# Kernel tuning notes

Measured on AMD Instinct MI355X. Metric: run time of the kernel, lower is better.

The kernel has to match this reference:

```python
import jax, jax.numpy as jnp
import numpy as np

N = 100000
E = 3200000
D = 128


def setup_inputs() -> dict:
    key = jax.random.key(0)
    k1, k2, k3, k4 = jax.random.split(key, 4)
    x = jax.random.normal(k1, (N, D), dtype=jnp.float32)
    edge_index = jax.random.randint(k2, (2, E), 0, N, dtype=jnp.int64)
    W1 = jax.random.normal(k3, (D, 16), dtype=jnp.float32) * (1.0 / np.sqrt(D))
    b1 = jnp.zeros((16,), dtype=jnp.float32)
    W2 = jax.random.normal(k4, (16, 2), dtype=jnp.float32) * (1.0 / np.sqrt(16))
    b2 = jnp.zeros((2,), dtype=jnp.float32)
    return {"x": x, "edge_index": edge_index, "W1": W1, "b1": b1, "W2": W2, "b2": b2}


def _gcn_conv(h, src, dst, norm, W, b):
    # transform first (out_dim <= in_dim), then normalized scatter-add aggregation
    h = h @ W                                   # [N, out]
    msg = h[src] * norm[:, None]                # [E+N, out] gathered messages
    agg = jax.ops.segment_sum(msg, dst, num_segments=N)
    return agg + b


def reference(x, edge_index, W1, b1, W2, b2):
    loops = jnp.arange(N, dtype=edge_index.dtype)
    src = jnp.concatenate([edge_index[0], loops])   # row (message source)
    dst = jnp.concatenate([edge_index[1], loops])   # col (aggregation target)
    # symmetric GCN normalization: deg over dst, norm = d^-1/2[src] * d^-1/2[dst]
    deg = jax.ops.segment_sum(jnp.ones_like(src, dtype=x.dtype), dst, num_segments=N)
    dinv = jnp.where(deg > 0, jax.lax.rsqrt(deg), 0.0)
    norm = dinv[src] * dinv[dst]

    h = _gcn_conv(x, src, dst, norm, W1, b1)
    h = jax.nn.relu(h)
    h = _gcn_conv(h, src, dst, norm, W2, b2)
    return jax.nn.log_softmax(h, axis=1)
```

## Files before the change

kernel.cpp:

```cpp
#include <hip/hip_runtime.h>
#include <hip/hip_fp16.h>
#include <math.h>

#define N_NODES 100000
#define N_EDGES 3200000
#define D_IN    128
#define H1      16

#define PSH     8
#define NPB     200
#define NB      500
#define CAP     9936
#define PBLK    512
#define CHUNK   6250
#define ELS_CAP 13760
#define NLINES  (ELS_CAP / 16)
#define MROWS   64

__device__ __forceinline__ unsigned bkt(int d) {
    return (unsigned)(((unsigned long long)(unsigned)d * 671089ull) >> 27);
}


__global__ __launch_bounds__(512) void k_partition(const int* __restrict__ ei,
                                                   int* __restrict__ cursor,
                                                   unsigned int* __restrict__ eop) {
    __shared__ int h[512];
    __shared__ int loff[512];
    __shared__ int resv[NB];
    __shared__ int wsum[8], wpre[8];
    __shared__ unsigned short owner[NLINES];
    __shared__ unsigned char rank8[CHUNK];
    __shared__ unsigned int els[ELS_CAP];
    int t = threadIdx.x;
    h[t] = 0;
    __syncthreads();
    int c0 = blockIdx.x * CHUNK;
    const int2* s2 = (const int2*)(ei + c0);
    const int2* d2 = (const int2*)(ei + N_EDGES + c0);
    for (int i = t; i < CHUNK / 2; i += 512) {
        int2 dd = d2[i];
        rank8[2 * i]     = (unsigned char)atomicAdd(&h[bkt(dd.x)], 1);
        rank8[2 * i + 1] = (unsigned char)atomicAdd(&h[bkt(dd.y)], 1);
    }
    __syncthreads();
    int cp = (h[t] + 15) & ~15;
    int lane = t & 63, w = t >> 6;
    int v = cp;
#pragma unroll
    for (int o = 1; o < 64; o <<= 1) {
        int u = __shfl_up(v, o);
        if (lane >= o) v += u;
    }
    if (lane == 63) wsum[w] = v;
    __syncthreads();
    if (t < 8) {
        int s = wsum[t];
#pragma unroll
        for (int o = 1; o < 8; o <<= 1) {
            int u = __shfl_up(s, o);
            if (t >= o) s += u;
        }
        wpre[t] = s;
    }
    __syncthreads();
    int inc = v + ((w > 0) ? wpre[w - 1] : 0);
    int totalpad = wpre[7];
    int ex = inc - cp;
    loff[t] = ex;
    if (t < NB && cp) {
        resv[t] = atomicAdd(&cursor[t], cp);
        int l0 = ex >> 4;
        for (int k = 0; k < (cp >> 4); ++k) owner[l0 + k] = (unsigned short)t;
    }
    for (int i = t; i < totalpad; i += 512) els[i] = 0xFFFFFFFFu;
    __syncthreads();
    for (int i = t; i < CHUNK / 2; i += 512) {
        int2 ss = s2[i];
        int2 dd = d2[i];
        unsigned bx = bkt(dd.x), by = bkt(dd.y);
        els[loff[bx] + (int)rank8[2 * i]] =
            ((unsigned)ss.x << PSH) | (unsigned)(dd.x - (int)(bx * NPB));
        els[loff[by] + (int)rank8[2 * i + 1]] =
            ((unsigned)ss.y << PSH) | (unsigned)(dd.y - (int)(by * NPB));
    }
    __syncthreads();
    for (int i = t; i < totalpad; i += 512) {
        int b   = owner[i >> 4];
        int pos = resv[b] + (i - loff[b]);
        if (pos < CAP)
            eop[(size_t)b * CAP + pos] = els[i];
    }
}

__global__ __launch_bounds__(512) void k_build(const int* __restrict__ cursor,
                                               unsigned int* __restrict__ eop,
                                               int* __restrict__ nstart,
                                               int* __restrict__ ndeg,
                                               float* __restrict__ dinv) {
    __shared__ unsigned int els[CAP];
    __shared__ int cnt[256];
    __shared__ int off[256];
    __shared__ int wsum[4], wpre[4];
    int t = threadIdx.x, b = blockIdx.x;
    if (t < 256) cnt[t] = 0;
    __syncthreads();
    int n = cursor[b]; if (n > CAP) n = CAP;
    unsigned int* reg = eop + (size_t)b * CAP;
    for (int i4 = t; i4 < (n >> 2); i4 += 512) {
        uint4 wv = ((const uint4*)reg)[i4];
        unsigned int e0 = wv.x, e1 = wv.y, e2 = wv.z, e3 = wv.w;
        int r;
        if ((int)e0 >= 0) { r = atomicAdd(&cnt[e0 & 0xFF], 1); e0 |= (unsigned)r << 25; }
        if ((int)e1 >= 0) { r = atomicAdd(&cnt[e1 & 0xFF], 1); e1 |= (unsigned)r << 25; }
        if ((int)e2 >= 0) { r = atomicAdd(&cnt[e2 & 0xFF], 1); e2 |= (unsigned)r << 25; }
        if ((int)e3 >= 0) { r = atomicAdd(&cnt[e3 & 0xFF], 1); e3 |= (unsigned)r << 25; }
        ((uint4*)els)[i4] = make_uint4(e0, e1, e2, e3);
    }
    __syncthreads();
    int lane = t & 63, w = t >> 6;
    int v = 0;
    if (t < 256) {
        v = cnt[t];
#pragma unroll
        for (int o = 1; o < 64; o <<= 1) {
            int u = __shfl_up(v, o);
            if (lane >= o) v += u;
        }
        if (lane == 63) wsum[w] = v;
    }
    __syncthreads();
    if (t < 4) {
        int s = wsum[t];
#pragma unroll
        for (int o = 1; o < 4; o <<= 1) {
            int u = __shfl_up(s, o);
            if (t >= o) s += u;
        }
        wpre[t] = s;
    }
    __syncthreads();
    if (t < 256) {
        int val = cnt[t];
        int ex = (v + ((w > 0) ? wpre[w - 1] : 0)) - val;
        off[t] = ex;
        if (t < NPB) {
            int node = b * NPB + t;
            nstart[node] = b * CAP + ex;
            ndeg[node]   = val;
            dinv[node]   = rsqrtf((float)(val + 1));
        }
    }
    __syncthreads();
    for (int i4 = t; i4 < (n >> 2); i4 += 512) {
        uint4 wv = ((const uint4*)els)[i4];
        unsigned int e; unsigned s;
        e = wv.x; s = (e >> PSH) & 0x1FFFFu;
        if (s < N_NODES) reg[off[e & 0xFF] + (int)(e >> 25)] = s;
        e = wv.y; s = (e >> PSH) & 0x1FFFFu;
        if (s < N_NODES) reg[off[e & 0xFF] + (int)(e >> 25)] = s;
        e = wv.z; s = (e >> PSH) & 0x1FFFFu;
        if (s < N_NODES) reg[off[e & 0xFF] + (int)(e >> 25)] = s;
        e = wv.w; s = (e >> PSH) & 0x1FFFFu;
        if (s < N_NODES) reg[off[e & 0xFF] + (int)(e >> 25)] = s;
    }
}

__global__ __launch_bounds__(256) void k_mm1(const float* __restrict__ x,
                                             const float* __restrict__ W1,
                                             const float* __restrict__ dinv,
                                             __half* __restrict__ h1h) {
    __shared__ float sX[MROWS][D_IN + 1];
    int t = threadIdx.x;
    int r0 = blockIdx.x * MROWS;
    for (int i = t; i < MROWS * (D_IN / 4); i += 256) {
        int row = i >> 5, c4 = i & 31;
        int grow = r0 + row;
        float4 v = (grow < N_NODES) ? ((const float4*)x)[(size_t)grow * 32 + c4]
                                    : make_float4(0.f, 0.f, 0.f, 0.f);
        sX[row][c4 * 4 + 0] = v.x; sX[row][c4 * 4 + 1] = v.y;
        sX[row][c4 * 4 + 2] = v.z; sX[row][c4 * 4 + 3] = v.w;
    }
    __syncthreads();
    int lane = t & 63;
    int c0 = __builtin_amdgcn_readfirstlane((t >> 6) * 4);
    float a0 = 0.f, a1 = 0.f, a2 = 0.f, a3 = 0.f;
#pragma unroll 4
    for (int d = 0; d < D_IN; ++d) {
        float xv = sX[lane][d];
        a0 = fmaf(xv, W1[d * 16 + c0 + 0], a0);
        a1 = fmaf(xv, W1[d * 16 + c0 + 1], a1);
        a2 = fmaf(xv, W1[d * 16 + c0 + 2], a2);
        a3 = fmaf(xv, W1[d * 16 + c0 + 3], a3);
    }
    int grow = r0 + lane;
    if (grow < N_NODES) {
        float di = dinv[grow];
        __half2* o = (__half2*)(h1h + (size_t)grow * H1 + c0);
        o[0] = __floats2half2_rn(a0 * di, a1 * di);
        o[1] = __floats2half2_rn(a2 * di, a3 * di);
    }
}

__global__ __launch_bounds__(256) void k_agg1(const unsigned int* __restrict__ eop,
                                              const int* __restrict__ nstart,
                                              const int* __restrict__ ndeg,
                                              const __half* __restrict__ h1h,
                                              const float* __restrict__ dinv,
                                              const float* __restrict__ b1,
                                              const float* __restrict__ W2,
                                              float2* __restrict__ h2f) {
    int t = threadIdx.x;
    int g = t >> 3, l = t & 7;
    int base = (t & 63) & ~7;
    int node = blockIdx.x * 32 + g;
    int e0 = nstart[node], deg = ndeg[node];
    const __half2* H = (const __half2*)h1h;
    float a0 = 0.f, a1 = 0.f, c0 = 0.f, c1 = 0.f;
    int nfull = deg & ~7;
    int j = e0;
    for (; j < e0 + nfull; j += 8) {
        int s = (int)eop[j + l];
#pragma unroll
        for (int k = 0; k < 8; k += 2) {
            int sk0 = __shfl(s, base + k);
            int sk1 = __shfl(s, base + k + 1);
            float2 f0 = __half22float2(H[sk0 * 8 + l]);
            float2 f1 = __half22float2(H[sk1 * 8 + l]);
            a0 += f0.x; a1 += f0.y;
            c0 += f1.x; c1 += f1.y;
        }
    }
    int r = e0 + deg - j;
    if (r) {
        int s = (l < r) ? (int)eop[j + l] : -1;
#pragma unroll
        for (int k = 0; k < 8; ++k) {
            int sk = __shfl(s, base + k);
            int su = (sk >= 0) ? sk : 0;
            float m = (sk >= 0) ? 1.f : 0.f;
            float2 f = __half22float2(H[su * 8 + l]);
            a0 = fmaf(f.x, m, a0); a1 = fmaf(f.y, m, a1);
        }
    }
    float di = dinv[node];
    float2 self = __half22float2(H[node * 8 + l]);
    float s0 = (a0 + c0) + self.x, s1 = (a1 + c1) + self.y;
    float2 bb = ((const float2*)b1)[l];
    float h0 = fmaxf(fmaf(di, s0, bb.x), 0.f);
    float h1v = fmaxf(fmaf(di, s1, bb.y), 0.f);
    float4 wv = ((const float4*)W2)[l];
    float p0 = h0 * wv.x + h1v * wv.z;
    float p1 = h0 * wv.y + h1v * wv.w;
#pragma unroll
    for (int off = 1; off < 8; off <<= 1) {
        p0 += __shfl_xor(p0, off);
        p1 += __shfl_xor(p1, off);
    }
    if (l == 0) h2f[node] = make_float2(p0 * di, p1 * di);
}

__global__ __launch_bounds__(256) void k_agg2(const unsigned int* __restrict__ eop,
                                              const int* __restrict__ nstart,
                                              const int* __restrict__ ndeg,
                                              const float2* __restrict__ h2f,
                                              const float* __restrict__ dinv,
                                              const float* __restrict__ b2,
                                              float* __restrict__ out) {
    int tg = blockIdx.x * 256 + threadIdx.x;
    int node = tg >> 2, l = tg & 3;
    if (node >= N_NODES) return;
    int e0 = nstart[node], e1 = e0 + ndeg[node];
    float ax = 0.f, ay = 0.f;
    for (int j = e0 + l; j < e1; j += 4) {
        float2 m = h2f[eop[j]];
        ax += m.x; ay += m.y;
    }
    ax += __shfl_xor(ax, 1); ay += __shfl_xor(ay, 1);
    ax += __shfl_xor(ax, 2); ay += __shfl_xor(ay, 2);
    if (l == 0) {
        float di = dinv[node];
        float2 self = h2f[node];
        float a0 = fmaf(di, ax + self.x, b2[0]);
        float a1 = fmaf(di, ay + self.y, b2[1]);
        float m  = fmaxf(a0, a1);
        float lg = logf(expf(a0 - m) + expf(a1 - m));
        out[2 * node]     = a0 - m - lg;
        out[2 * node + 1] = a1 - m - lg;
    }
}

extern "C" void kernel_launch(void* const* d_in, const int* in_sizes, int n_in,
                              void* d_out, int out_size, void* d_ws, size_t ws_size,
                              hipStream_t stream) {
    const float* x  = (const float*)d_in[0];
    const int*   ei = (const int*)d_in[1];
    const float* W1 = (const float*)d_in[2];
    const float* b1 = (const float*)d_in[3];
    const float* W2 = (const float*)d_in[4];
    const float* b2 = (const float*)d_in[5];
    float* out = (float*)d_out;

    int*          cursor = (int*)d_ws;
    int*          nstart = cursor + 512;
    int*          ndeg   = nstart + 100352;
    float*        dinv   = (float*)(ndeg + 100352);
    __half*       h1h    = (__half*)(dinv + 100352);
    float2*       h2f    = (float2*)(h1h + (size_t)100352 * H1);
    unsigned int* eop    = (unsigned int*)(h2f + 100352);

    hipMemsetAsync(cursor, 0, 512 * sizeof(int), stream);
    k_partition<<<PBLK, 512, 0, stream>>>(ei, cursor, eop);
    k_build    <<<NB,   512, 0, stream>>>(cursor, eop, nstart, ndeg, dinv);
    k_mm1      <<<(N_NODES + MROWS - 1) / MROWS, 256, 0, stream>>>(x, W1, dinv, h1h);
    k_agg1     <<<N_NODES / 32, 256, 0, stream>>>(eop, nstart, ndeg, h1h, dinv, b1, W2, h2f);
    k_agg2     <<<(N_NODES * 4 + 255) / 256, 256, 0, stream>>>(eop, nstart, ndeg, h2f, dinv, b2, out);
}
```

Before: 204.0 us.

## Fuse partition and build into one cooperative kernel with grid sync

Merges the edge-partition and per-bucket build kernels into a single cooperative kernel. A grid-wide barrier now separates the two phases instead of a kernel boundary, and both phases share one shared-memory union. The aim is to remove one launch and its inter-kernel gap. In exchange, all 512 blocks must be co-resident, and the grid sync plus the raised occupancy hint may cost some throughput.

```diff
diff --git a/kernel.cpp b/kernel.cpp
--- a/kernel.cpp
+++ b/kernel.cpp
@@ -1,6 +1,9 @@
 #include <hip/hip_runtime.h>
+#include <hip/hip_cooperative_groups.h>
 #include <hip/hip_fp16.h>
 #include <math.h>
+
+namespace cg = cooperative_groups;
 
 #define N_NODES 100000
 #define N_EDGES 3200000
@@ -22,147 +25,159 @@
 }
 
 
-__global__ __launch_bounds__(512) void k_partition(const int* __restrict__ ei,
-                                                   int* __restrict__ cursor,
-                                                   unsigned int* __restrict__ eop) {
-    __shared__ int h[512];
-    __shared__ int loff[512];
-    __shared__ int resv[NB];
-    __shared__ int wsum[8], wpre[8];
-    __shared__ unsigned short owner[NLINES];
-    __shared__ unsigned char rank8[CHUNK];
-    __shared__ unsigned int els[ELS_CAP];
+struct PShared {
+    int h[512];
+    int loff[512];
+    int resv[NB];
+    int wsum[8], wpre[8];
+    unsigned short owner[NLINES];
+    unsigned char rank8[CHUNK];
+    unsigned int els[ELS_CAP];
+};
+struct BShared {
+    unsigned int els[CAP];
+    int cnt[256];
+    int off[256];
+    int wsum[4], wpre[4];
+};
+union SortShared { PShared p; BShared b; };
+
+__global__ __launch_bounds__(512, 4) void k_sort(const int* __restrict__ ei,
+                                                 int* __restrict__ cursor,
+                                                 unsigned int* __restrict__ eop,
+                                                 int* __restrict__ nstart,
+                                                 int* __restrict__ ndeg,
+                                                 float* __restrict__ dinv) {
+    __shared__ SortShared sm;
     int t = threadIdx.x;
-    h[t] = 0;
-    __syncthreads();
-    int c0 = blockIdx.x * CHUNK;
-    const int2* s2 = (const int2*)(ei + c0);
-    const int2* d2 = (const int2*)(ei + N_EDGES + c0);
-    for (int i = t; i < CHUNK / 2; i += 512) {
-        int2 dd = d2[i];
-        rank8[2 * i]     = (unsigned char)atomicAdd(&h[bkt(dd.x)], 1);
-        rank8[2 * i + 1] = (unsigned char)atomicAdd(&h[bkt(dd.y)], 1);
-    }
-    __syncthreads();
-    int cp = (h[t] + 15) & ~15;
-    int lane = t & 63, w = t >> 6;
-    int v = cp;
-#pragma unroll
-    for (int o = 1; o < 64; o <<= 1) {
-        int u = __shfl_up(v, o);
-        if (lane >= o) v += u;
-    }
-    if (lane == 63) wsum[w] = v;
-    __syncthreads();
-    if (t < 8) {
-        int s = wsum[t];
-#pragma unroll
-        for (int o = 1; o < 8; o <<= 1) {
-            int u = __shfl_up(s, o);
-            if (t >= o) s += u;
-        }
-        wpre[t] = s;
-    }
-    __syncthreads();
-    int inc = v + ((w > 0) ? wpre[w - 1] : 0);
-    int totalpad = wpre[7];
-    int ex = inc - cp;
-    loff[t] = ex;
-    if (t < NB && cp) {
-        resv[t] = atomicAdd(&cursor[t], cp);
-        int l0 = ex >> 4;
-        for (int k = 0; k < (cp >> 4); ++k) owner[l0 + k] = (unsigned short)t;
-    }
-    for (int i = t; i < totalpad; i += 512) els[i] = 0xFFFFFFFFu;
-    __syncthreads();
-    for (int i = t; i < CHUNK / 2; i += 512) {
-        int2 ss = s2[i];
-        int2 dd = d2[i];
-        unsigned bx = bkt(dd.x), by = bkt(dd.y);
-        els[loff[bx] + (int)rank8[2 * i]] =
-            ((unsigned)ss.x << PSH) | (unsigned)(dd.x - (int)(bx * NPB));
-        els[loff[by] + (int)rank8[2 * i + 1]] =
-            ((unsigned)ss.y << PSH) | (unsigned)(dd.y - (int)(by * NPB));
-    }
-    __syncthreads();
-    for (int i = t; i < totalpad; i += 512) {
-        int b   = owner[i >> 4];
-        int pos = resv[b] + (i - loff[b]);
-        if (pos < CAP)
-            eop[(size_t)b * CAP + pos] = els[i];
-    }
-}
-
-__global__ __launch_bounds__(512) void k_build(const int* __restrict__ cursor,
-                                               unsigned int* __restrict__ eop,
-                                               int* __restrict__ nstart,
-                                               int* __restrict__ ndeg,
-                                               float* __restrict__ dinv) {
-    __shared__ unsigned int els[CAP];
-    __shared__ int cnt[256];
-    __shared__ int off[256];
-    __shared__ int wsum[4], wpre[4];
-    int t = threadIdx.x, b = blockIdx.x;
-    if (t < 256) cnt[t] = 0;
-    __syncthreads();
-    int n = cursor[b]; if (n > CAP) n = CAP;
-    unsigned int* reg = eop + (size_t)b * CAP;
-    for (int i4 = t; i4 < (n >> 2); i4 += 512) {
-        uint4 wv = ((const uint4*)reg)[i4];
-        unsigned int e0 = wv.x, e1 = wv.y, e2 = wv.z, e3 = wv.w;
-        int r;
-        if ((int)e0 >= 0) { r = atomicAdd(&cnt[e0 & 0xFF], 1); e0 |= (unsigned)r << 25; }
-        if ((int)e1 >= 0) { r = atomicAdd(&cnt[e1 & 0xFF], 1); e1 |= (unsigned)r << 25; }
-        if ((int)e2 >= 0) { r = atomicAdd(&cnt[e2 & 0xFF], 1); e2 |= (unsigned)r << 25; }
-        if ((int)e3 >= 0) { r = atomicAdd(&cnt[e3 & 0xFF], 1); e3 |= (unsigned)r << 25; }
-        ((uint4*)els)[i4] = make_uint4(e0, e1, e2, e3);
-    }
-    __syncthreads();
-    int lane = t & 63, w = t >> 6;
-    int v = 0;
-    if (t < 256) {
-        v = cnt[t];
+
+    {
+        sm.p.h[t] = 0;
+        __syncthreads();
+        int c0 = blockIdx.x * CHUNK;
+        const int2* s2 = (const int2*)(ei + c0);
+        const int2* d2 = (const int2*)(ei + N_EDGES + c0);
+        for (int i = t; i < CHUNK / 2; i += 512) {
+            int2 dd = d2[i];
+            sm.p.rank8[2 * i]     = (unsigned char)atomicAdd(&sm.p.h[bkt(dd.x)], 1);
+            sm.p.rank8[2 * i + 1] = (unsigned char)atomicAdd(&sm.p.h[bkt(dd.y)], 1);
+        }
+        __syncthreads();
+        int cp = (sm.p.h[t] + 15) & ~15;
+        int lane = t & 63, w = t >> 6;
+        int v = cp;
 #pragma unroll
         for (int o = 1; o < 64; o <<= 1) {
             int u = __shfl_up(v, o);
             if (lane >= o) v += u;
         }
-        if (lane == 63) wsum[w] = v;
-    }
-    __syncthreads();
-    if (t < 4) {
-        int s = wsum[t];
-#pragma unroll
-        for (int o = 1; o < 4; o <<= 1) {
-            int u = __shfl_up(s, o);
-            if (t >= o) s += u;
-        }
-        wpre[t] = s;
-    }
-    __syncthreads();
-    if (t < 256) {
-        int val = cnt[t];
-        int ex = (v + ((w > 0) ? wpre[w - 1] : 0)) - val;
-        off[t] = ex;
-        if (t < NPB) {
-            int node = b * NPB + t;
-            nstart[node] = b * CAP + ex;
-            ndeg[node]   = val;
-            dinv[node]   = rsqrtf((float)(val + 1));
-        }
-    }
-    __syncthreads();
-    for (int i4 = t; i4 < (n >> 2); i4 += 512) {
-        uint4 wv = ((const uint4*)els)[i4];
-        unsigned int e; unsigned s;
-        e = wv.x; s = (e >> PSH) & 0x1FFFFu;
-        if (s < N_NODES) reg[off[e & 0xFF] + (int)(e >> 25)] = s;
-        e = wv.y; s = (e >> PSH) & 0x1FFFFu;
-        if (s < N_NODES) reg[off[e & 0xFF] + (int)(e >> 25)] = s;
-        e = wv.z; s = (e >> PSH) & 0x1FFFFu;
-        if (s < N_NODES) reg[off[e & 0xFF] + (int)(e >> 25)] = s;
-        e = wv.w; s = (e >> PSH) & 0x1FFFFu;
-        if (s < N_NODES) reg[off[e & 0xFF] + (int)(e >> 25)] = s;
+        if (lane == 63) sm.p.wsum[w] = v;
+        __syncthreads();
+        if (t < 8) {
+            int s = sm.p.wsum[t];
+#pragma unroll
+            for (int o = 1; o < 8; o <<= 1) {
+                int u = __shfl_up(s, o);
+                if (t >= o) s += u;
+            }
+            sm.p.wpre[t] = s;
+        }
+        __syncthreads();
+        int inc = v + ((w > 0) ? sm.p.wpre[w - 1] : 0);
+        int totalpad = sm.p.wpre[7];
+        int ex = inc - cp;
+        sm.p.loff[t] = ex;
+        if (t < NB && cp) {
+            sm.p.resv[t] = atomicAdd(&cursor[t], cp);
+            int l0 = ex >> 4;
+            for (int k = 0; k < (cp >> 4); ++k) sm.p.owner[l0 + k] = (unsigned short)t;
+        }
+        for (int i = t; i < totalpad; i += 512) sm.p.els[i] = 0xFFFFFFFFu;
+        __syncthreads();
+        for (int i = t; i < CHUNK / 2; i += 512) {
+            int2 ss = s2[i];
+            int2 dd = d2[i];
+            unsigned bx = bkt(dd.x), by = bkt(dd.y);
+            sm.p.els[sm.p.loff[bx] + (int)sm.p.rank8[2 * i]] =
+                ((unsigned)ss.x << PSH) | (unsigned)(dd.x - (int)(bx * NPB));
+            sm.p.els[sm.p.loff[by] + (int)sm.p.rank8[2 * i + 1]] =
+                ((unsigned)ss.y << PSH) | (unsigned)(dd.y - (int)(by * NPB));
+        }
+        __syncthreads();
+        for (int i = t; i < totalpad; i += 512) {
+            int b   = sm.p.owner[i >> 4];
+            int pos = sm.p.resv[b] + (i - sm.p.loff[b]);
+            if (pos < CAP)
+                eop[(size_t)b * CAP + pos] = sm.p.els[i];
+        }
+    }
+
+    __threadfence();
+    cg::this_grid().sync();
+
+    int b = blockIdx.x;
+    if (b < NB) {
+        if (t < 256) sm.b.cnt[t] = 0;
+        __syncthreads();
+        int n = cursor[b]; if (n > CAP) n = CAP;
+        unsigned int* reg = eop + (size_t)b * CAP;
+        for (int i4 = t; i4 < (n >> 2); i4 += 512) {
+            uint4 wv = ((const uint4*)reg)[i4];
+            unsigned int e0 = wv.x, e1 = wv.y, e2 = wv.z, e3 = wv.w;
+            int r;
+            if ((int)e0 >= 0) { r = atomicAdd(&sm.b.cnt[e0 & 0xFF], 1); e0 |= (unsigned)r << 25; }
+            if ((int)e1 >= 0) { r = atomicAdd(&sm.b.cnt[e1 & 0xFF], 1); e1 |= (unsigned)r << 25; }
+            if ((int)e2 >= 0) { r = atomicAdd(&sm.b.cnt[e2 & 0xFF], 1); e2 |= (unsigned)r << 25; }
+            if ((int)e3 >= 0) { r = atomicAdd(&sm.b.cnt[e3 & 0xFF], 1); e3 |= (unsigned)r << 25; }
+            ((uint4*)sm.b.els)[i4] = make_uint4(e0, e1, e2, e3);
+        }
+        __syncthreads();
+        int lane = t & 63, w = t >> 6;
+        int v = 0;
+        if (t < 256) {
+            v = sm.b.cnt[t];
+#pragma unroll
+            for (int o = 1; o < 64; o <<= 1) {
+                int u = __shfl_up(v, o);
+                if (lane >= o) v += u;
+            }
+            if (lane == 63) sm.b.wsum[w] = v;
+        }
+        __syncthreads();
+        if (t < 4) {
+            int s = sm.b.wsum[t];
+#pragma unroll
+            for (int o = 1; o < 4; o <<= 1) {
+                int u = __shfl_up(s, o);
+                if (t >= o) s += u;
+            }
+            sm.b.wpre[t] = s;
+        }
+        __syncthreads();
+        if (t < 256) {
+            int val = sm.b.cnt[t];
+            int ex = (v + ((w > 0) ? sm.b.wpre[w - 1] : 0)) - val;
+            sm.b.off[t] = ex;
+            if (t < NPB) {
+                int node = b * NPB + t;
+                nstart[node] = b * CAP + ex;
+                ndeg[node]   = val;
+                dinv[node]   = rsqrtf((float)(val + 1));
+            }
+        }
+        __syncthreads();
+        for (int i4 = t; i4 < (n >> 2); i4 += 512) {
+            uint4 wv = ((const uint4*)sm.b.els)[i4];
+            unsigned int e; unsigned s;
+            e = wv.x; s = (e >> PSH) & 0x1FFFFu;
+            if (s < N_NODES) reg[sm.b.off[e & 0xFF] + (int)(e >> 25)] = s;
+            e = wv.y; s = (e >> PSH) & 0x1FFFFu;
+            if (s < N_NODES) reg[sm.b.off[e & 0xFF] + (int)(e >> 25)] = s;
+            e = wv.z; s = (e >> PSH) & 0x1FFFFu;
+            if (s < N_NODES) reg[sm.b.off[e & 0xFF] + (int)(e >> 25)] = s;
+            e = wv.w; s = (e >> PSH) & 0x1FFFFu;
+            if (s < N_NODES) reg[sm.b.off[e & 0xFF] + (int)(e >> 25)] = s;
+        }
     }
 }
 
@@ -310,9 +325,17 @@
     unsigned int* eop    = (unsigned int*)(h2f + 100352);
 
     hipMemsetAsync(cursor, 0, 512 * sizeof(int), stream);
-    k_partition<<<PBLK, 512, 0, stream>>>(ei, cursor, eop);
-    k_build    <<<NB,   512, 0, stream>>>(cursor, eop, nstart, ndeg, dinv);
-    k_mm1      <<<(N_NODES + MROWS - 1) / MROWS, 256, 0, stream>>>(x, W1, dinv, h1h);
-    k_agg1     <<<N_NODES / 32, 256, 0, stream>>>(eop, nstart, ndeg, h1h, dinv, b1, W2, h2f);
-    k_agg2     <<<(N_NODES * 4 + 255) / 256, 256, 0, stream>>>(eop, nstart, ndeg, h2f, dinv, b2, out);
-}
+
+    {
+        const int*    a0 = ei;     int*   a1 = cursor;
+        unsigned int* a2 = eop;    int*   a3 = nstart;
+        int*          a4 = ndeg;   float* a5 = dinv;
+        void* ka[6] = { &a0, &a1, &a2, &a3, &a4, &a5 };
+        hipLaunchCooperativeKernel((const void*)k_sort, dim3(PBLK), dim3(512),
+                                   ka, 0, stream);
+    }
+
+    k_mm1 <<<(N_NODES + MROWS - 1) / MROWS, 256, 0, stream>>>(x, W1, dinv, h1h);
+    k_agg1<<<N_NODES / 32, 256, 0, stream>>>(eop, nstart, ndeg, h1h, dinv, b1, W2, h2f);
+    k_agg2<<<(N_NODES * 4 + 255) / 256, 256, 0, stream>>>(eop, nstart, ndeg, h2f, dinv, b2, out);
+}
```

Measured after the change: 350.1 us. 1.72x slower.

## Fuse X·W1 into partition kernel, apply dinv during aggregation, pad cursors

Applied to the files above, without the earlier changes.

The separate k_mm1 kernel is removed. The dense X·W1 product now runs at the tail of k_partition, reusing its shared-memory buffer, with each block handling 196 rows. The product is stored without the dinv scaling, since dinv is not known until k_build, so k_agg1 now gathers dinv[src] per edge and multiplies it in. Cursor counters are spread 32 ints apart to reduce atomic contention, and k_agg2 uses 8 lanes per node instead of 4. The trade is one fewer launch and overlap of the GEMM with partitioning, against an extra scattered dinv load per edge in agg1 and a longer partition kernel.

```diff
diff --git a/kernel.cpp b/kernel.cpp
--- a/kernel.cpp
+++ b/kernel.cpp
@@ -15,7 +15,8 @@
 #define CHUNK   6250
 #define ELS_CAP 13760
 #define NLINES  (ELS_CAP / 16)
-#define MROWS   64
+#define CSTRIDE 32
+#define MMR     196
 
 __device__ __forceinline__ unsigned bkt(int d) {
     return (unsigned)(((unsigned long long)(unsigned)d * 671089ull) >> 27);
@@ -24,7 +25,10 @@
 
 __global__ __launch_bounds__(512) void k_partition(const int* __restrict__ ei,
                                                    int* __restrict__ cursor,
-                                                   unsigned int* __restrict__ eop) {
+                                                   unsigned int* __restrict__ eop,
+                                                   const float* __restrict__ x,
+                                                   const float* __restrict__ W1,
+                                                   __half* __restrict__ h1u) {
     __shared__ int h[512];
     __shared__ int loff[512];
     __shared__ int resv[NB];
@@ -35,9 +39,9 @@
     int t = threadIdx.x;
     h[t] = 0;
     __syncthreads();
-    int c0 = blockIdx.x * CHUNK;
-    const int2* s2 = (const int2*)(ei + c0);
-    const int2* d2 = (const int2*)(ei + N_EDGES + c0);
+    int c0e = blockIdx.x * CHUNK;
+    const int2* s2 = (const int2*)(ei + c0e);
+    const int2* d2 = (const int2*)(ei + N_EDGES + c0e);
     for (int i = t; i < CHUNK / 2; i += 512) {
         int2 dd = d2[i];
         rank8[2 * i]     = (unsigned char)atomicAdd(&h[bkt(dd.x)], 1);
@@ -69,7 +73,7 @@
     int ex = inc - cp;
     loff[t] = ex;
     if (t < NB && cp) {
-        resv[t] = atomicAdd(&cursor[t], cp);
+        resv[t] = atomicAdd(&cursor[t * CSTRIDE], cp);
         int l0 = ex >> 4;
         for (int k = 0; k < (cp >> 4); ++k) owner[l0 + k] = (unsigned short)t;
     }
@@ -90,6 +94,35 @@
         int pos = resv[b] + (i - loff[b]);
         if (pos < CAP)
             eop[(size_t)b * CAP + pos] = els[i];
+    }
+
+    float (*sXf)[D_IN + 1] = (float (*)[D_IN + 1])els;
+    int cc = __builtin_amdgcn_readfirstlane(2 * w);
+    int rbase = blockIdx.x * MMR;
+    for (int p = 0; p < 4; ++p) {
+        int pb = rbase + p * 64;
+        __syncthreads();
+        for (int i = t; i < 64 * 32; i += 512) {
+            int row = i >> 5, c4 = i & 31;
+            int grow = pb + row;
+            float4 vv = (grow < N_NODES) ? ((const float4*)x)[(size_t)grow * 32 + c4]
+                                         : make_float4(0.f, 0.f, 0.f, 0.f);
+            sXf[row][c4 * 4 + 0] = vv.x; sXf[row][c4 * 4 + 1] = vv.y;
+            sXf[row][c4 * 4 + 2] = vv.z; sXf[row][c4 * 4 + 3] = vv.w;
+        }
+        __syncthreads();
+        int lrow = p * 64 + lane;
+        int grow = pb + lane;
+        if (lrow < MMR && grow < N_NODES) {
+            float a0 = 0.f, a1 = 0.f;
+#pragma unroll 4
+            for (int d = 0; d < D_IN; ++d) {
+                float xv = sXf[lane][d];
+                a0 = fmaf(xv, W1[d * 16 + cc], a0);
+                a1 = fmaf(xv, W1[d * 16 + cc + 1], a1);
+            }
+            ((__half2*)h1u)[(size_t)grow * 8 + w] = __floats2half2_rn(a0, a1);
+        }
     }
 }
 
@@ -105,7 +138,7 @@
     int t = threadIdx.x, b = blockIdx.x;
     if (t < 256) cnt[t] = 0;
     __syncthreads();
-    int n = cursor[b]; if (n > CAP) n = CAP;
+    int n = cursor[b * CSTRIDE]; if (n > CAP) n = CAP;
     unsigned int* reg = eop + (size_t)b * CAP;
     for (int i4 = t; i4 < (n >> 2); i4 += 512) {
         uint4 wv = ((const uint4*)reg)[i4];
@@ -166,46 +199,10 @@
     }
 }
 
-__global__ __launch_bounds__(256) void k_mm1(const float* __restrict__ x,
-                                             const float* __restrict__ W1,
-                                             const float* __restrict__ dinv,
-                                             __half* __restrict__ h1h) {
-    __shared__ float sX[MROWS][D_IN + 1];
-    int t = threadIdx.x;
-    int r0 = blockIdx.x * MROWS;
-    for (int i = t; i < MROWS * (D_IN / 4); i += 256) {
-        int row = i >> 5, c4 = i & 31;
-        int grow = r0 + row;
-        float4 v = (grow < N_NODES) ? ((const float4*)x)[(size_t)grow * 32 + c4]
-                                    : make_float4(0.f, 0.f, 0.f, 0.f);
-        sX[row][c4 * 4 + 0] = v.x; sX[row][c4 * 4 + 1] = v.y;
-        sX[row][c4 * 4 + 2] = v.z; sX[row][c4 * 4 + 3] = v.w;
-    }
-    __syncthreads();
-    int lane = t & 63;
-    int c0 = __builtin_amdgcn_readfirstlane((t >> 6) * 4);
-    float a0 = 0.f, a1 = 0.f, a2 = 0.f, a3 = 0.f;
-#pragma unroll 4
-    for (int d = 0; d < D_IN; ++d) {
-        float xv = sX[lane][d];
-        a0 = fmaf(xv, W1[d * 16 + c0 + 0], a0);
-        a1 = fmaf(xv, W1[d * 16 + c0 + 1], a1);
-        a2 = fmaf(xv, W1[d * 16 + c0 + 2], a2);
-        a3 = fmaf(xv, W1[d * 16 + c0 + 3], a3);
-    }
-    int grow = r0 + lane;
-    if (grow < N_NODES) {
-        float di = dinv[grow];
-        __half2* o = (__half2*)(h1h + (size_t)grow * H1 + c0);
-        o[0] = __floats2half2_rn(a0 * di, a1 * di);
-        o[1] = __floats2half2_rn(a2 * di, a3 * di);
-    }
-}
-
 __global__ __launch_bounds__(256) void k_agg1(const unsigned int* __restrict__ eop,
                                               const int* __restrict__ nstart,
                                               const int* __restrict__ ndeg,
-                                              const __half* __restrict__ h1h,
+                                              const __half* __restrict__ h1u,
                                               const float* __restrict__ dinv,
                                               const float* __restrict__ b1,
                                               const float* __restrict__ W2,
@@ -215,7 +212,7 @@
     int base = (t & 63) & ~7;
     int node = blockIdx.x * 32 + g;
     int e0 = nstart[node], deg = ndeg[node];
-    const __half2* H = (const __half2*)h1h;
+    const __half2* H = (const __half2*)h1u;
     float a0 = 0.f, a1 = 0.f, c0 = 0.f, c1 = 0.f;
     int nfull = deg & ~7;
     int j = e0;
@@ -225,10 +222,12 @@
         for (int k = 0; k < 8; k += 2) {
             int sk0 = __shfl(s, base + k);
             int sk1 = __shfl(s, base + k + 1);
+            float dv0 = dinv[sk0];
+            float dv1 = dinv[sk1];
             float2 f0 = __half22float2(H[sk0 * 8 + l]);
             float2 f1 = __half22float2(H[sk1 * 8 + l]);
-            a0 += f0.x; a1 += f0.y;
-            c0 += f1.x; c1 += f1.y;
+            a0 = fmaf(f0.x, dv0, a0); a1 = fmaf(f0.y, dv0, a1);
+            c0 = fmaf(f1.x, dv1, c0); c1 = fmaf(f1.y, dv1, c1);
         }
     }
     int r = e0 + deg - j;
@@ -238,14 +237,14 @@
         for (int k = 0; k < 8; ++k) {
             int sk = __shfl(s, base + k);
             int su = (sk >= 0) ? sk : 0;
-            float m = (sk >= 0) ? 1.f : 0.f;
+            float dv = (sk >= 0) ? dinv[su] : 0.f;
             float2 f = __half22float2(H[su * 8 + l]);
-            a0 = fmaf(f.x, m, a0); a1 = fmaf(f.y, m, a1);
+            a0 = fmaf(f.x, dv, a0); a1 = fmaf(f.y, dv, a1);
         }
     }
     float di = dinv[node];
     float2 self = __half22float2(H[node * 8 + l]);
-    float s0 = (a0 + c0) + self.x, s1 = (a1 + c1) + self.y;
+    float s0 = (a0 + c0) + self.x * di, s1 = (a1 + c1) + self.y * di;
     float2 bb = ((const float2*)b1)[l];
     float h0 = fmaxf(fmaf(di, s0, bb.x), 0.f);
     float h1v = fmaxf(fmaf(di, s1, bb.y), 0.f);
@@ -268,16 +267,16 @@
                                               const float* __restrict__ b2,
                                               float* __restrict__ out) {
     int tg = blockIdx.x * 256 + threadIdx.x;
-    int node = tg >> 2, l = tg & 3;
-    if (node >= N_NODES) return;
+    int node = tg >> 3, l = tg & 7;
     int e0 = nstart[node], e1 = e0 + ndeg[node];
     float ax = 0.f, ay = 0.f;
-    for (int j = e0 + l; j < e1; j += 4) {
+    for (int j = e0 + l; j < e1; j += 8) {
         float2 m = h2f[eop[j]];
         ax += m.x; ay += m.y;
     }
     ax += __shfl_xor(ax, 1); ay += __shfl_xor(ay, 1);
     ax += __shfl_xor(ax, 2); ay += __shfl_xor(ay, 2);
+    ax += __shfl_xor(ax, 4); ay += __shfl_xor(ay, 4);
     if (l == 0) {
         float di = dinv[node];
         float2 self = h2f[node];
@@ -302,17 +301,17 @@
     float* out = (float*)d_out;
 
     int*          cursor = (int*)d_ws;
-    int*          nstart = cursor + 512;
+    int*          nstart = cursor + 16384;
     int*          ndeg   = nstart + 100352;
     float*        dinv   = (float*)(ndeg + 100352);
-    __half*       h1h    = (__half*)(dinv + 100352);
-    float2*       h2f    = (float2*)(h1h + (size_t)100352 * H1);
+    __half*       h1u    = (__half*)(dinv + 100352);
+    float2*       h2f    = (float2*)(h1u + (size_t)100352 * H1);
     unsigned int* eop    = (unsigned int*)(h2f + 100352);
 
-    hipMemsetAsync(cursor, 0, 512 * sizeof(int), stream);
-    k_partition<<<PBLK, 512, 0, stream>>>(ei, cursor, eop);
+    hipMemsetAsync(cursor, 0, 16384 * sizeof(int), stream);
+
+    k_partition<<<PBLK, 512, 0, stream>>>(ei, cursor, eop, x, W1, h1u);
     k_build    <<<NB,   512, 0, stream>>>(cursor, eop, nstart, ndeg, dinv);
-    k_mm1      <<<(N_NODES + MROWS - 1) / MROWS, 256, 0, stream>>>(x, W1, dinv, h1h);
-    k_agg1     <<<N_NODES / 32, 256, 0, stream>>>(eop, nstart, ndeg, h1h, dinv, b1, W2, h2f);
-    k_agg2     <<<(N_NODES * 4 + 255) / 256, 256, 0, stream>>>(eop, nstart, ndeg, h2f, dinv, b2, out);
-}
+    k_agg1     <<<N_NODES / 32, 256, 0, stream>>>(eop, nstart, ndeg, h1u, dinv, b1, W2, h2f);
+    k_agg2     <<<N_NODES / 32, 256, 0, stream>>>(eop, nstart, ndeg, h2f, dinv, b2, out);
+}
```

New measurement: 223.8 us. +9.7%, slower.

## Widen agg1 gathers to 8-byte loads, regroup agg2 lanes, pad partition cursors

Applied to the files above, without the earlier changes.

The first aggregation kernel now uses 4 lanes per node, and each lane gathers a float2 (four halves), in place of 8 lanes each loading one half2. This halves the lanes per node and doubles the bytes per load, so each wavefront covers twice as many nodes. The second aggregation now uses 8 lanes per node instead of 4, and the per-bucket atomic cursors are padded to a 32-int stride to avoid contention on shared cache lines. The trade-offs are more serial edge iterations per lane in agg1, and the removal of the bounds check in agg2, which relies on N being divisible by 32.

```diff
diff --git a/kernel.cpp b/kernel.cpp
--- a/kernel.cpp
+++ b/kernel.cpp
@@ -15,6 +15,7 @@
 #define CHUNK   6250
 #define ELS_CAP 13760
 #define NLINES  (ELS_CAP / 16)
+#define CSTRIDE 32
 #define MROWS   64
 
 __device__ __forceinline__ unsigned bkt(int d) {
@@ -69,7 +70,7 @@
     int ex = inc - cp;
     loff[t] = ex;
     if (t < NB && cp) {
-        resv[t] = atomicAdd(&cursor[t], cp);
+        resv[t] = atomicAdd(&cursor[t * CSTRIDE], cp);
         int l0 = ex >> 4;
         for (int k = 0; k < (cp >> 4); ++k) owner[l0 + k] = (unsigned short)t;
     }
@@ -105,7 +106,7 @@
     int t = threadIdx.x, b = blockIdx.x;
     if (t < 256) cnt[t] = 0;
     __syncthreads();
-    int n = cursor[b]; if (n > CAP) n = CAP;
+    int n = cursor[b * CSTRIDE]; if (n > CAP) n = CAP;
     unsigned int* reg = eop + (size_t)b * CAP;
     for (int i4 = t; i4 < (n >> 2); i4 += 512) {
         uint4 wv = ((const uint4*)reg)[i4];
@@ -211,52 +212,64 @@
                                               const float* __restrict__ W2,
                                               float2* __restrict__ h2f) {
     int t = threadIdx.x;
-    int g = t >> 3, l = t & 7;
-    int base = (t & 63) & ~7;
-    int node = blockIdx.x * 32 + g;
+    int g = t >> 2, l = t & 3;
+    int base = (t & 63) & ~3;
+    int node = blockIdx.x * 64 + g;
+    if (node >= N_NODES) return;
     int e0 = nstart[node], deg = ndeg[node];
-    const __half2* H = (const __half2*)h1h;
-    float a0 = 0.f, a1 = 0.f, c0 = 0.f, c1 = 0.f;
-    int nfull = deg & ~7;
+    const float2* H = (const float2*)h1h;
+    float a0 = 0.f, a1 = 0.f, a2 = 0.f, a3 = 0.f;
+    float c0 = 0.f, c1 = 0.f, c2 = 0.f, c3 = 0.f;
+    int nfull = deg & ~3;
     int j = e0;
-    for (; j < e0 + nfull; j += 8) {
+    for (; j < e0 + nfull; j += 4) {
         int s = (int)eop[j + l];
 #pragma unroll
-        for (int k = 0; k < 8; k += 2) {
+        for (int k = 0; k < 4; k += 2) {
             int sk0 = __shfl(s, base + k);
             int sk1 = __shfl(s, base + k + 1);
-            float2 f0 = __half22float2(H[sk0 * 8 + l]);
-            float2 f1 = __half22float2(H[sk1 * 8 + l]);
-            a0 += f0.x; a1 += f0.y;
-            c0 += f1.x; c1 += f1.y;
+            float2 r0 = H[sk0 * 4 + l];
+            float2 r1 = H[sk1 * 4 + l];
+            float2 f00 = __half22float2(*(const __half2*)&r0.x);
+            float2 f01 = __half22float2(*(const __half2*)&r0.y);
+            float2 f10 = __half22float2(*(const __half2*)&r1.x);
+            float2 f11 = __half22float2(*(const __half2*)&r1.y);
+            a0 += f00.x; a1 += f00.y; a2 += f01.x; a3 += f01.y;
+            c0 += f10.x; c1 += f10.y; c2 += f11.x; c3 += f11.y;
         }
     }
     int r = e0 + deg - j;
     if (r) {
         int s = (l < r) ? (int)eop[j + l] : -1;
 #pragma unroll
-        for (int k = 0; k < 8; ++k) {
+        for (int k = 0; k < 4; ++k) {
             int sk = __shfl(s, base + k);
             int su = (sk >= 0) ? sk : 0;
             float m = (sk >= 0) ? 1.f : 0.f;
-            float2 f = __half22float2(H[su * 8 + l]);
-            a0 = fmaf(f.x, m, a0); a1 = fmaf(f.y, m, a1);
+            float2 rr = H[su * 4 + l];
+            float2 f0 = __half22float2(*(const __half2*)&rr.x);
+            float2 f1 = __half22float2(*(const __half2*)&rr.y);
+            a0 = fmaf(f0.x, m, a0); a1 = fmaf(f0.y, m, a1);
+            a2 = fmaf(f1.x, m, a2); a3 = fmaf(f1.y, m, a3);
         }
     }
     float di = dinv[node];
-    float2 self = __half22float2(H[node * 8 + l]);
-    float s0 = (a0 + c0) + self.x, s1 = (a1 + c1) + self.y;
-    float2 bb = ((const float2*)b1)[l];
+    float2 sr = H[node * 4 + l];
+    float2 s01 = __half22float2(*(const __half2*)&sr.x);
+    float2 s23 = __half22float2(*(const __half2*)&sr.y);
+    float s0 = (a0 + c0) + s01.x, s1 = (a1 + c1) + s01.y;
+    float s2 = (a2 + c2) + s23.x, s3 = (a3 + c3) + s23.y;
+    float4 bb = ((const float4*)b1)[l];
     float h0 = fmaxf(fmaf(di, s0, bb.x), 0.f);
     float h1v = fmaxf(fmaf(di, s1, bb.y), 0.f);
-    float4 wv = ((const float4*)W2)[l];
-    float p0 = h0 * wv.x + h1v * wv.z;
-    float p1 = h0 * wv.y + h1v * wv.w;
-#pragma unroll
-    for (int off = 1; off < 8; off <<= 1) {
-        p0 += __shfl_xor(p0, off);
-        p1 += __shfl_xor(p1, off);
-    }
+    float h2v = fmaxf(fmaf(di, s2, bb.z), 0.f);
+    float h3v = fmaxf(fmaf(di, s3, bb.w), 0.f);
+    float4 wa = ((const float4*)W2)[2 * l];
+    float4 wb = ((const float4*)W2)[2 * l + 1];
+    float p0 = h0 * wa.x + h1v * wa.z + h2v * wb.x + h3v * wb.z;
+    float p1 = h0 * wa.y + h1v * wa.w + h2v * wb.y + h3v * wb.w;
+    p0 += __shfl_xor(p0, 1); p1 += __shfl_xor(p1, 1);
+    p0 += __shfl_xor(p0, 2); p1 += __shfl_xor(p1, 2);
     if (l == 0) h2f[node] = make_float2(p0 * di, p1 * di);
 }
 
@@ -268,16 +281,16 @@
                                               const float* __restrict__ b2,
                                               float* __restrict__ out) {
     int tg = blockIdx.x * 256 + threadIdx.x;
-    int node = tg >> 2, l = tg & 3;
-    if (node >= N_NODES) return;
+    int node = tg >> 3, l = tg & 7;
     int e0 = nstart[node], e1 = e0 + ndeg[node];
     float ax = 0.f, ay = 0.f;
-    for (int j = e0 + l; j < e1; j += 4) {
+    for (int j = e0 + l; j < e1; j += 8) {
         float2 m = h2f[eop[j]];
         ax += m.x; ay += m.y;
     }
     ax += __shfl_xor(ax, 1); ay += __shfl_xor(ay, 1);
     ax += __shfl_xor(ax, 2); ay += __shfl_xor(ay, 2);
+    ax += __shfl_xor(ax, 4); ay += __shfl_xor(ay, 4);
     if (l == 0) {
         float di = dinv[node];
         float2 self = h2f[node];
@@ -302,17 +315,18 @@
     float* out = (float*)d_out;
 
     int*          cursor = (int*)d_ws;
-    int*          nstart = cursor + 512;
+    int*          nstart = cursor + 16384;
     int*          ndeg   = nstart + 100352;
     float*        dinv   = (float*)(ndeg + 100352);
     __half*       h1h    = (__half*)(dinv + 100352);
     float2*       h2f    = (float2*)(h1h + (size_t)100352 * H1);
     unsigned int* eop    = (unsigned int*)(h2f + 100352);
 
-    hipMemsetAsync(cursor, 0, 512 * sizeof(int), stream);
+    hipMemsetAsync(cursor, 0, 16384 * sizeof(int), stream);
+
     k_partition<<<PBLK, 512, 0, stream>>>(ei, cursor, eop);
     k_build    <<<NB,   512, 0, stream>>>(cursor, eop, nstart, ndeg, dinv);
     k_mm1      <<<(N_NODES + MROWS - 1) / MROWS, 256, 0, stream>>>(x, W1, dinv, h1h);
-    k_agg1     <<<N_NODES / 32, 256, 0, stream>>>(eop, nstart, ndeg, h1h, dinv, b1, W2, h2f);
-    k_agg2     <<<(N_NODES * 4 + 255) / 256, 256, 0, stream>>>(eop, nstart, ndeg, h2f, dinv, b2, out);
-}
+    k_agg1     <<<(N_NODES + 63) / 64, 256, 0, stream>>>(eop, nstart, ndeg, h1h, dinv, b1, W2, h2f);
+    k_agg2     <<<N_NODES / 32, 256, 0, stream>>>(eop, nstart, ndeg, h2f, dinv, b2, out);
+}
```

New measurement: 211.0 us. 1.03x slower.
